# Kernel optimization log

Measured on AMD Instinct MI355X. Metric: run time of the kernel, lower is better.

The kernel has to match this reference:

```python
import jax, jax.numpy as jnp
import numpy as np

B, L, R, A, E = 256, 64, 1024, 512, 1024


def lstm_cell(x, h, c, W_ih, W_hh, b_ih, b_hh):
    # PyTorch LSTMCell gate order: i, f, g, o
    gates = x @ W_ih.T + b_ih + h @ W_hh.T + b_hh
    i, f, g, o = jnp.split(gates, 4, axis=1)
    c2 = jax.nn.sigmoid(f) * c + jax.nn.sigmoid(i) * jnp.tanh(g)
    h2 = jax.nn.sigmoid(o) * jnp.tanh(c2)
    return h2, c2


def attend(h, wh_w, wh_b, wa_w, wa_b, feats_proj, feats_value):
    # Bahdanau attention: tanh(Wh h + proj(feats)) -> scalar logit -> softmax -> weighted sum
    dot = jnp.tanh(feats_proj + (h @ wh_w.T + wh_b)[:, None, :])  # [B,L,A]
    logits = jnp.einsum('bla,a->bl', dot, wa_w[0]) + wa_b[0]      # [B,L]
    w = jax.nn.softmax(logits, axis=1)
    return jnp.einsum('bl,bld->bd', w, feats_value)


def setup_inputs() -> dict:
    key = jax.random.key(0)
    ks = iter(jax.random.split(key, 64))
    rn = lambda shape, s=1.0: jax.random.normal(next(ks), shape, dtype=jnp.float32) * s
    inp = {
        'xt': rn((B, E)),
        'fc_feats': rn((B, R)),
        'roi_feats': rn((B, L, R)),
        'p_roi_feats': rn((B, L, A)),
        'context_feats': rn((B, L, R)),
        'state_h': rn((2, B, R)),
        'state_c': rn((2, B, R)),
        # scco (visual) LSTM: input E + 2R
        'W_ih_v': rn((4 * R, E + 2 * R), 0.02), 'W_hh_v': rn((4 * R, R), 0.02),
        'b_ih_v': rn((4 * R,), 0.02), 'b_hh_v': rn((4 * R,), 0.02),
        # language LSTM: input 2R
        'W_ih_l': rn((4 * R, 2 * R), 0.02), 'W_hh_l': rn((4 * R, R), 0.02),
        'b_ih_l': rn((4 * R,), 0.02), 'b_hh_l': rn((4 * R,), 0.02),
        # SingleSP: wh, wa
        'sp_wh_w': rn((A, R), 0.02), 'sp_wh_b': rn((A,), 0.02),
        'sp_wa_w': rn((1, A), 0.02), 'sp_wa_b': rn((1,), 0.02),
        # ContextSP: wh, wv, wa
        'ctx_wh_w': rn((A, R), 0.02), 'ctx_wh_b': rn((A,), 0.02),
        'ctx_wv_w': rn((A, R), 0.02), 'ctx_wv_b': rn((A,), 0.02),
        'ctx_wa_w': rn((1, A), 0.02), 'ctx_wa_b': rn((1,), 0.02),
        # CompSP: wh, wv, wa
        'cmp_wh_w': rn((A, R), 0.02), 'cmp_wh_b': rn((A,), 0.02),
        'cmp_wv_w': rn((A, R), 0.02), 'cmp_wv_b': rn((A,), 0.02),
        'cmp_wa_w': rn((1, A), 0.02), 'cmp_wa_b': rn((1,), 0.02),
        # OutputSP: wv, wh, wa
        'out_wv_w': rn((A, R), 0.02), 'out_wv_b': rn((A,), 0.02),
        'out_wh_w': rn((A, R), 0.02), 'out_wh_b': rn((A,), 0.02),
        'out_wa_w': rn((1, A), 0.02), 'out_wa_b': rn((1,), 0.02),
    }
    return inp


def reference(xt, fc_feats, roi_feats, p_roi_feats, context_feats, state_h, state_c,
              W_ih_v, W_hh_v, b_ih_v, b_hh_v, W_ih_l, W_hh_l, b_ih_l, b_hh_l,
              sp_wh_w, sp_wh_b, sp_wa_w, sp_wa_b,
              ctx_wh_w, ctx_wh_b, ctx_wv_w, ctx_wv_b, ctx_wa_w, ctx_wa_b,
              cmp_wh_w, cmp_wh_b, cmp_wv_w, cmp_wv_b, cmp_wa_w, cmp_wa_b,
              out_wv_w, out_wv_b, out_wh_w, out_wh_b, out_wa_w, out_wa_b):
    prev_h = state_h[-1]
    env = jnp.concatenate([prev_h, fc_feats, xt], axis=1)  # [B, 2R+E]
    h_vis, c_vis = lstm_cell(env, state_h[0], state_c[0], W_ih_v, W_hh_v, b_ih_v, b_hh_v)

    # SingleSP: attend over rois using precomputed projections p_roi_feats
    single_feat = attend(h_vis, sp_wh_w, sp_wh_b, sp_wa_w, sp_wa_b, p_roi_feats, roi_feats)

    # ContextSP: attend over context_feats
    ctx_proj = context_feats @ ctx_wv_w.T + ctx_wv_b
    context_feat = attend(h_vis, ctx_wh_w, ctx_wh_b, ctx_wa_w, ctx_wa_b, ctx_proj, context_feats)

    # CompSP: attend over relation feats = context - roi
    rel = context_feat[:, None, :] - roi_feats  # [B,L,R]
    rel_proj = rel @ cmp_wv_w.T + cmp_wv_b
    comp_feat = attend(h_vis, cmp_wh_w, cmp_wh_b, cmp_wa_w, cmp_wa_b, rel_proj, rel)

    # OutputSP: attend over {single, comp, fc}
    feats3 = jnp.stack([single_feat, comp_feat, fc_feats], axis=1)  # [B,3,R]
    f3_proj = feats3 @ out_wv_w.T + out_wv_b
    output_feats = attend(h_vis, out_wh_w, out_wh_b, out_wa_w, out_wa_b, f3_proj, feats3)

    lang_in = jnp.concatenate([output_feats, h_vis], axis=1)  # [B,2R]
    h_lang, c_lang = lstm_cell(lang_in, state_h[1], state_c[1], W_ih_l, W_hh_l, b_ih_l, b_hh_l)

    output = h_lang  # dropout is identity in eval mode
    new_h = jnp.stack([h_vis, h_lang])
    new_c = jnp.stack([c_vis, c_lang])
    return output, new_h, new_c, output_feats
```

## Files before the change

### kernel.cpp

```cpp
#include <hip/hip_runtime.h>
#include <hip/hip_bf16.h>
#include <math.h>

#define B_ 256
#define L_ 64
#define R_ 1024
#define A_ 512
#define E_ 1024
#define BR (B_ * R_)

typedef __attribute__((ext_vector_type(8))) short short8;
typedef __attribute__((ext_vector_type(4))) float f32x4;

__device__ __forceinline__ unsigned int pkbf(float x, float y) {
    union { __hip_bfloat162 h; unsigned int u; } cv;
    cv.h = __float22bfloat162_rn(make_float2(x, y));
    return cv.u;
}

__device__ __forceinline__ float tanh_fast(float x) {
    return 1.f - 2.f / (1.f + __expf(2.f * x));
}
__device__ __forceinline__ float sigm_(float x) { return 1.f / (1.f + __expf(-x)); }

__device__ __forceinline__ void mm_core(const float* __restrict__ Abm, int lda,
                                        const float* __restrict__ Wbn, int ldw,
                                        int K, f32x4 acc[4][4])
{
    __shared__ unsigned int As[2048];
    __shared__ unsigned int Ws[2048];

    const int t = threadIdx.x;
    const int srow = t >> 3;
    const int sub = t & 7;
    const int q = sub >> 1, half = sub & 1;
    const int csw = (q ^ ((srow >> 1) & 3));
    int sidx[4];
    const float* pa[4];
    const float* pw[4];
    #pragma unroll
    for (int i = 0; i < 4; ++i) {
        int row = srow + 32 * i;
        sidx[i] = row * 16 + csw * 4 + half * 2;
        pa[i] = Abm + (size_t)row * lda + sub * 4;
        pw[i] = Wbn + (size_t)row * ldw + sub * 4;
    }

    const int w = t >> 6, lane = t & 63;
    const int m0 = (w >> 1) * 64, n0 = (w & 1) * 64;
    const int lrow = lane & 15, quad = lane >> 4;
    int aidx[4], widx[4];
    #pragma unroll
    for (int i = 0; i < 4; ++i) {
        int ra = m0 + i * 16 + lrow;
        aidx[i] = ra * 16 + ((quad ^ ((ra >> 1) & 3)) << 2);
        int rw = n0 + i * 16 + lrow;
        widx[i] = rw * 16 + ((quad ^ ((rw >> 1) & 3)) << 2);
    }

    for (int k0 = 0; k0 < K; k0 += 32) {
        #pragma unroll
        for (int i = 0; i < 4; ++i) {
            float4 av = *(const float4*)pa[i]; pa[i] += 32;
            float4 wv = *(const float4*)pw[i]; pw[i] += 32;
            *(uint2*)(As + sidx[i]) = make_uint2(pkbf(av.x, av.y), pkbf(av.z, av.w));
            *(uint2*)(Ws + sidx[i]) = make_uint2(pkbf(wv.x, wv.y), pkbf(wv.z, wv.w));
        }
        __syncthreads();
        short8 af[4], wf[4];
        #pragma unroll
        for (int i = 0; i < 4; ++i) {
            af[i] = *(const short8*)(As + aidx[i]);
            wf[i] = *(const short8*)(Ws + widx[i]);
        }
        #pragma unroll
        for (int mt = 0; mt < 4; ++mt)
            #pragma unroll
            for (int nt = 0; nt < 4; ++nt)
                acc[mt][nt] = __builtin_amdgcn_mfma_f32_16x16x32_bf16(
                    af[mt], wf[nt], acc[mt][nt], 0, 0, 0);
        __syncthreads();
    }
}

__device__ __forceinline__ void mm_store(f32x4 acc[4][4], float* Cbm, int ldc,
                                         int bn, const float* bias)
{
    const int t = threadIdx.x;
    const int w = t >> 6, lane = t & 63;
    const int m0 = (w >> 1) * 64, n0 = (w & 1) * 64;
    const int lrow = lane & 15, quad = lane >> 4;
    #pragma unroll
    for (int nt = 0; nt < 4; ++nt) {
        int col = bn + n0 + nt * 16 + lrow;
        float bv = bias ? bias[col] : 0.f;
        #pragma unroll
        for (int mt = 0; mt < 4; ++mt) {
            int rbase = m0 + mt * 16 + quad * 4;
            #pragma unroll
            for (int r = 0; r < 4; ++r)
                Cbm[(size_t)(rbase + r) * ldc + col] = acc[mt][nt][r] + bv;
        }
    }
}

__global__ __launch_bounds__(256) void mm_plain(
    const float* __restrict__ A, int lda, const float* __restrict__ W, int ldw,
    const float* __restrict__ bias, float* __restrict__ C, int ldc, int K,
    int M1, const float* __restrict__ A2, const float* __restrict__ bias2,
    float* __restrict__ C2)
{
    int bm = blockIdx.y * 128, bn = blockIdx.x * 128;
    const float* Abm; float* Cbm; const float* bs;
    if (bm < M1) {
        Abm = A + (size_t)bm * lda; Cbm = C + (size_t)bm * ldc; bs = bias;
    } else {
        int bm2 = bm - M1;
        Abm = A2 + (size_t)bm2 * lda; Cbm = C2 + (size_t)bm2 * ldc; bs = bias2;
    }
    f32x4 acc[4][4];
    #pragma unroll
    for (int i = 0; i < 4; ++i)
        #pragma unroll
        for (int j = 0; j < 4; ++j) acc[i][j] = (f32x4)0.f;
    mm_core(Abm, lda, W + (size_t)bn * ldw, ldw, K, acc);
    mm_store(acc, Cbm, ldc, bn, bs);
}

struct P4 { const float* W[4]; const float* bias[4]; };
__global__ __launch_bounds__(256) void mm_batch4(
    const float* __restrict__ A, int lda, P4 p, float* __restrict__ Cbase,
    int ldc, int K, int zstride)
{
    int z = blockIdx.z;
    int bm = blockIdx.y * 128, bn = blockIdx.x * 128;
    f32x4 acc[4][4];
    #pragma unroll
    for (int i = 0; i < 4; ++i)
        #pragma unroll
        for (int j = 0; j < 4; ++j) acc[i][j] = (f32x4)0.f;
    mm_core(A + (size_t)bm * lda, lda, p.W[z] + (size_t)bn * lda, lda, K, acc);
    mm_store(acc, Cbase + (size_t)z * zstride + (size_t)bm * ldc, ldc, bn, p.bias[z]);
}

struct C4 { const float* A[4]; const float* W[4]; int lda[4]; int ldw[4]; };
__global__ __launch_bounds__(256) void mm_chunks(
    C4 p, float* __restrict__ Cbase, int ldc, int K, int zstride)
{
    int z = blockIdx.z;
    int bm = blockIdx.y * 128, bn = blockIdx.x * 128;
    f32x4 acc[4][4];
    #pragma unroll
    for (int i = 0; i < 4; ++i)
        #pragma unroll
        for (int j = 0; j < 4; ++j) acc[i][j] = (f32x4)0.f;
    mm_core(p.A[z] + (size_t)bm * p.lda[z], p.lda[z],
            p.W[z] + (size_t)bn * p.ldw[z], p.ldw[z], K, acc);
    mm_store(acc, Cbase + (size_t)z * zstride + (size_t)bm * ldc, ldc, bn, nullptr);
}

__global__ void build_env(const float* __restrict__ prev_h,
                          const float* __restrict__ fc,
                          const float* __restrict__ xt,
                          float* __restrict__ env)
{
    int idx = blockIdx.x * blockDim.x + threadIdx.x;
    int b = idx / 3072, k = idx - b * 3072;
    float v;
    if (k < R_)          v = prev_h[b * R_ + k];
    else if (k < 2 * R_) v = fc[b * R_ + (k - R_)];
    else                 v = xt[b * E_ + (k - 2 * R_)];
    env[idx] = v;
}

__global__ void build_lang_in(const float* __restrict__ of,
                              const float* __restrict__ hv,
                              float* __restrict__ li)
{
    int idx = blockIdx.x * blockDim.x + threadIdx.x;
    int b = idx >> 11, k = idx & 2047;
    li[idx] = (k < R_) ? of[b * R_ + k] : hv[b * R_ + (k - R_)];
}

__global__ void build_feats3(const float* __restrict__ sf,
                             const float* __restrict__ cf,
                             const float* __restrict__ fc,
                             float* __restrict__ f3)
{
    int idx = blockIdx.x * blockDim.x + threadIdx.x;
    int d = idx % R_;
    int tt = idx / R_;
    int j = tt % 3, b = tt / 3;
    float v;
    if (j == 0)      v = sf[b * R_ + d];
    else if (j == 1) v = cf[b * R_ + d];
    else             v = fc[b * R_ + d];
    f3[idx] = v;
}

__global__ void lstm_pw(const float* __restrict__ gp, int P,
                        const float* __restrict__ b_ih, const float* __restrict__ b_hh,
                        const float* __restrict__ c_prev,
                        float* __restrict__ h_out, float* __restrict__ h_out2,
                        float* __restrict__ c_out)
{
    int idx = blockIdx.x * blockDim.x + threadIdx.x;
    int b = idx >> 10, r = idx & (R_ - 1);
    float g[4];
    #pragma unroll
    for (int gi = 0; gi < 4; ++gi) {
        int o = gi * R_ + r;
        float s = b_ih[o] + b_hh[o];
        for (int p = 0; p < P; ++p)
            s += gp[(size_t)p * B_ * 4096 + (size_t)b * 4096 + o];
        g[gi] = s;
    }
    float c2 = sigm_(g[1]) * c_prev[idx] + sigm_(g[0]) * tanh_fast(g[2]);
    float h2 = sigm_(g[3]) * tanh_fast(c2);
    c_out[idx] = c2;
    h_out[idx] = h2;
    if (h_out2) h_out2[idx] = h2;
}

__global__ __launch_bounds__(256) void attn_logits(
    const float* __restrict__ base, const float* __restrict__ base2,
    const float* __restrict__ proj,
    const float* __restrict__ wa, const float* __restrict__ wa_b,
    float* __restrict__ logits, int L, float sign)
{
    int idx = blockIdx.x * 4 + (threadIdx.x >> 6);
    int lane = threadIdx.x & 63;
    int b = idx / L;
    const float* p = proj + (size_t)idx * A_;
    const float* bs = base + (size_t)b * A_;
    const float* bs2 = base2 ? base2 + (size_t)b * A_ : nullptr;
    float acc = 0.f;
    #pragma unroll
    for (int a0 = 0; a0 < A_; a0 += 64) {
        int a = a0 + lane;
        float bb = bs[a];
        if (bs2) bb += bs2[a];
        acc += tanh_fast(bb + sign * p[a]) * wa[a];
    }
    #pragma unroll
    for (int off = 32; off > 0; off >>= 1) acc += __shfl_xor(acc, off);
    if (lane == 0) logits[idx] = acc + wa_b[0];
}

__global__ __launch_bounds__(256) void softmax_rows(
    const float* __restrict__ logits, float* __restrict__ w, int L)
{
    int row = blockIdx.x * 4 + (threadIdx.x >> 6);
    int lane = threadIdx.x & 63;
    float v = (lane < L) ? logits[row * L + lane] : -INFINITY;
    float m = v;
    #pragma unroll
    for (int off = 32; off > 0; off >>= 1) m = fmaxf(m, __shfl_xor(m, off));
    float e = (lane < L) ? __expf(v - m) : 0.f;
    float s = e;
    #pragma unroll
    for (int off = 32; off > 0; off >>= 1) s += __shfl_xor(s, off);
    if (lane < L) w[row * L + lane] = e / s;
}

__global__ void weighted_sum(const float* __restrict__ w,
                             const float* __restrict__ V,
                             const float* __restrict__ addfrom,
                             float* __restrict__ out, int L, int D)
{
    int idx = blockIdx.x * blockDim.x + threadIdx.x;
    int b = idx / D, d = idx - b * D;
    const float* vp = V + (size_t)b * L * D + d;
    const float* wp = w + b * L;
    float acc = 0.f;
    for (int l = 0; l < L; ++l) acc += wp[l] * vp[(size_t)l * D];
    out[idx] = addfrom ? (addfrom[idx] - acc) : acc;
}

extern "C" void kernel_launch(void* const* d_in, const int* in_sizes, int n_in,
                              void* d_out, int out_size, void* d_ws, size_t ws_size,
                              hipStream_t stream)
{
    const float* xt      = (const float*)d_in[0];
    const float* fc      = (const float*)d_in[1];
    const float* roi     = (const float*)d_in[2];
    const float* p_roi   = (const float*)d_in[3];
    const float* ctxf    = (const float*)d_in[4];
    const float* sh      = (const float*)d_in[5];
    const float* sc      = (const float*)d_in[6];
    const float* W_ih_v  = (const float*)d_in[7];
    const float* W_hh_v  = (const float*)d_in[8];
    const float* b_ih_v  = (const float*)d_in[9];
    const float* b_hh_v  = (const float*)d_in[10];
    const float* W_ih_l  = (const float*)d_in[11];
    const float* W_hh_l  = (const float*)d_in[12];
    const float* b_ih_l  = (const float*)d_in[13];
    const float* b_hh_l  = (const float*)d_in[14];
    const float* sp_wh_w = (const float*)d_in[15];
    const float* sp_wh_b = (const float*)d_in[16];
    const float* sp_wa_w = (const float*)d_in[17];
    const float* sp_wa_b = (const float*)d_in[18];
    const float* ctx_wh_w= (const float*)d_in[19];
    const float* ctx_wh_b= (const float*)d_in[20];
    const float* ctx_wv_w= (const float*)d_in[21];
    const float* ctx_wv_b= (const float*)d_in[22];
    const float* ctx_wa_w= (const float*)d_in[23];
    const float* ctx_wa_b= (const float*)d_in[24];
    const float* cmp_wh_w= (const float*)d_in[25];
    const float* cmp_wh_b= (const float*)d_in[26];
    const float* cmp_wv_w= (const float*)d_in[27];
    const float* cmp_wv_b= (const float*)d_in[28];
    const float* cmp_wa_w= (const float*)d_in[29];
    const float* cmp_wa_b= (const float*)d_in[30];
    const float* out_wv_w= (const float*)d_in[31];
    const float* out_wv_b= (const float*)d_in[32];
    const float* out_wh_w= (const float*)d_in[33];
    const float* out_wh_b= (const float*)d_in[34];
    const float* out_wa_w= (const float*)d_in[35];
    const float* out_wa_b= (const float*)d_in[36];

    float* out = (float*)d_out;
    float* h_vis    = out + BR;
    float* h_lang   = out;
    float* h_lang2  = out + 2 * BR;
    float* c_vis    = out + 3 * BR;
    float* c_lang   = out + 4 * BR;
    float* out_feats= out + 5 * BR;

    float* ws = (float*)d_ws;
    float* env        = ws;
    float* proj_big   = env + (size_t)B_ * 3072;
    float* gates      = proj_big;
    float* hproj4     = proj_big + (size_t)16384 * A_;
    float* base_cmp2  = hproj4 + (size_t)4 * B_ * A_;
    float* logits     = base_cmp2 + (size_t)B_ * A_;
    float* attw       = logits + B_ * L_;
    float* single_feat= attw + B_ * L_;
    float* context_feat = single_feat + BR;
    float* comp_feat  = context_feat + BR;
    float* feats3     = comp_feat + BR;
    float* f3_proj    = feats3 + (size_t)B_ * 3 * R_;
    float* lang_in    = f3_proj + (size_t)768 * A_;

    const dim3 blk(256);
    const int HUGE_M = 1 << 30;

    build_env<<<dim3(B_ * 3072 / 256), blk, 0, stream>>>(sh + BR, fc, xt, env);
    {
        C4 cv;
        cv.A[0] = env;        cv.lda[0] = 3072; cv.W[0] = W_ih_v;        cv.ldw[0] = 3072;
        cv.A[1] = env + 1024; cv.lda[1] = 3072; cv.W[1] = W_ih_v + 1024; cv.ldw[1] = 3072;
        cv.A[2] = env + 2048; cv.lda[2] = 3072; cv.W[2] = W_ih_v + 2048; cv.ldw[2] = 3072;
        cv.A[3] = sh;         cv.lda[3] = 1024; cv.W[3] = W_hh_v;        cv.ldw[3] = 1024;
        mm_chunks<<<dim3(32, 2, 4), blk, 0, stream>>>(cv, gates, 4096, 1024, B_ * 4096);
    }
    lstm_pw<<<dim3(BR / 256), blk, 0, stream>>>(gates, 4, b_ih_v, b_hh_v, sc, h_vis, nullptr, c_vis);

    {
        P4 p;
        p.W[0] = sp_wh_w;  p.bias[0] = sp_wh_b;
        p.W[1] = ctx_wh_w; p.bias[1] = ctx_wh_b;
        p.W[2] = cmp_wh_w; p.bias[2] = cmp_wh_b;
        p.W[3] = out_wh_w; p.bias[3] = out_wh_b;
        mm_batch4<<<dim3(4, 2, 4), blk, 0, stream>>>(h_vis, 1024, p, hproj4, 512, 1024, B_ * A_);
    }

    attn_logits<<<dim3(B_ * L_ / 4), blk, 0, stream>>>(hproj4, nullptr, p_roi, sp_wa_w, sp_wa_b, logits, L_, 1.f);
    softmax_rows<<<dim3(B_ / 4), blk, 0, stream>>>(logits, attw, L_);
    weighted_sum<<<dim3(BR / 256), blk, 0, stream>>>(attw, roi, nullptr, single_feat, L_, R_);

    mm_plain<<<dim3(4, 128), blk, 0, stream>>>(ctxf, 1024, ctx_wv_w, 1024, ctx_wv_b,
                                               proj_big, 512, 1024, HUGE_M, nullptr, nullptr, nullptr);
    attn_logits<<<dim3(B_ * L_ / 4), blk, 0, stream>>>(hproj4 + (size_t)B_ * A_, nullptr, proj_big,
                                                       ctx_wa_w, ctx_wa_b, logits, L_, 1.f);
    softmax_rows<<<dim3(B_ / 4), blk, 0, stream>>>(logits, attw, L_);
    weighted_sum<<<dim3(BR / 256), blk, 0, stream>>>(attw, ctxf, nullptr, context_feat, L_, R_);

    mm_plain<<<dim3(4, 130), blk, 0, stream>>>(roi, 1024, cmp_wv_w, 1024, nullptr,
                                               proj_big, 512, 1024, 16384,
                                               context_feat, cmp_wv_b, base_cmp2);
    attn_logits<<<dim3(B_ * L_ / 4), blk, 0, stream>>>(hproj4 + (size_t)2 * B_ * A_, base_cmp2, proj_big,
                                                       cmp_wa_w, cmp_wa_b, logits, L_, -1.f);
    softmax_rows<<<dim3(B_ / 4), blk, 0, stream>>>(logits, attw, L_);
    weighted_sum<<<dim3(BR / 256), blk, 0, stream>>>(attw, roi, context_feat, comp_feat, L_, R_);

    build_feats3<<<dim3(B_ * 3 * R_ / 256), blk, 0, stream>>>(single_feat, comp_feat, fc, feats3);
    mm_plain<<<dim3(4, 6), blk, 0, stream>>>(feats3, 1024, out_wv_w, 1024, out_wv_b,
                                             f3_proj, 512, 1024, HUGE_M, nullptr, nullptr, nullptr);
    attn_logits<<<dim3(B_ * 3 / 4), blk, 0, stream>>>(hproj4 + (size_t)3 * B_ * A_, nullptr, f3_proj,
                                                      out_wa_w, out_wa_b, logits, 3, 1.f);
    softmax_rows<<<dim3(B_ / 4), blk, 0, stream>>>(logits, attw, 3);
    weighted_sum<<<dim3(BR / 256), blk, 0, stream>>>(attw, feats3, nullptr, out_feats, 3, R_);

    build_lang_in<<<dim3(B_ * 2048 / 256), blk, 0, stream>>>(out_feats, h_vis, lang_in);
    {
        C4 cl;
        cl.A[0] = lang_in;        cl.lda[0] = 2048; cl.W[0] = W_ih_l;        cl.ldw[0] = 2048;
        cl.A[1] = lang_in + 1024; cl.lda[1] = 2048; cl.W[1] = W_ih_l + 1024; cl.ldw[1] = 2048;
        cl.A[2] = sh + BR;        cl.lda[2] = 1024; cl.W[2] = W_hh_l;        cl.ldw[2] = 1024;
        cl.A[3] = sh + BR;        cl.lda[3] = 1024; cl.W[3] = W_hh_l;        cl.ldw[3] = 1024;
        mm_chunks<<<dim3(32, 2, 3), blk, 0, stream>>>(cl, gates, 4096, 1024, B_ * 4096);
    }
    lstm_pw<<<dim3(BR / 256), blk, 0, stream>>>(gates, 3, b_ih_l, b_hh_l, sc + BR, h_lang, h_lang2, c_lang);
}
```

Measured before the change: 718.3 us.

## Fuse attention logits into projection GEMMs, double-buffer LDS, split-K LSTM GEMMs

The GEMM core now double-buffers shared memory and prefetches the next K-slice into registers, so each iteration needs one barrier instead of two. The big context and relation projection GEMMs gain an epilogue that applies tanh and the wa dot product directly, writing per-column-tile partial logits. This removes the 16384x512 projection writes and their re-reads. The concatenation kernels are dropped in favour of split-K segments that read the inputs in place. Weighted sums are vectorised, and roi is read once to produce both the single and comp features. The cost is more partial-sum buffers and extra reduction work in lstm_pw and softmax.

```diff
diff --git a/kernel.cpp b/kernel.cpp
--- a/kernel.cpp
+++ b/kernel.cpp
@@ -27,30 +27,28 @@
                                         const float* __restrict__ Wbn, int ldw,
                                         int K, f32x4 acc[4][4])
 {
-    __shared__ unsigned int As[2048];
-    __shared__ unsigned int Ws[2048];
+    __shared__ unsigned int As[2][2048];
+    __shared__ unsigned int Ws[2][2048];
 
     const int t = threadIdx.x;
-    const int srow = t >> 3;
-    const int sub = t & 7;
-    const int q = sub >> 1, half = sub & 1;
-    const int csw = (q ^ ((srow >> 1) & 3));
+    const int srow = t >> 3, sub = t & 7;
+    const int half = sub & 1;
+    const int csw = (sub >> 1) ^ ((srow >> 1) & 3);
     int sidx[4];
     const float* pa[4];
     const float* pw[4];
-    #pragma unroll
+#pragma unroll
     for (int i = 0; i < 4; ++i) {
         int row = srow + 32 * i;
         sidx[i] = row * 16 + csw * 4 + half * 2;
         pa[i] = Abm + (size_t)row * lda + sub * 4;
         pw[i] = Wbn + (size_t)row * ldw + sub * 4;
     }
-
     const int w = t >> 6, lane = t & 63;
     const int m0 = (w >> 1) * 64, n0 = (w & 1) * 64;
     const int lrow = lane & 15, quad = lane >> 4;
     int aidx[4], widx[4];
-    #pragma unroll
+#pragma unroll
     for (int i = 0; i < 4; ++i) {
         int ra = m0 + i * 16 + lrow;
         aidx[i] = ra * 16 + ((quad ^ ((ra >> 1) & 3)) << 2);
@@ -58,144 +56,254 @@
         widx[i] = rw * 16 + ((quad ^ ((rw >> 1) & 3)) << 2);
     }
 
-    for (int k0 = 0; k0 < K; k0 += 32) {
-        #pragma unroll
-        for (int i = 0; i < 4; ++i) {
-            float4 av = *(const float4*)pa[i]; pa[i] += 32;
-            float4 wv = *(const float4*)pw[i]; pw[i] += 32;
-            *(uint2*)(As + sidx[i]) = make_uint2(pkbf(av.x, av.y), pkbf(av.z, av.w));
-            *(uint2*)(Ws + sidx[i]) = make_uint2(pkbf(wv.x, wv.y), pkbf(wv.z, wv.w));
-        }
+    float4 ra4[4], rw4[4];
+#define MMC_LOAD() do { _Pragma("unroll") for (int i = 0; i < 4; ++i) { \
+        ra4[i] = *(const float4*)pa[i]; rw4[i] = *(const float4*)pw[i]; \
+        pa[i] += 32; pw[i] += 32; } } while (0)
+#define MMC_STORE(buf) do { _Pragma("unroll") for (int i = 0; i < 4; ++i) { \
+        *(uint2*)(As[buf] + sidx[i]) = make_uint2(pkbf(ra4[i].x, ra4[i].y), pkbf(ra4[i].z, ra4[i].w)); \
+        *(uint2*)(Ws[buf] + sidx[i]) = make_uint2(pkbf(rw4[i].x, rw4[i].y), pkbf(rw4[i].z, rw4[i].w)); } } while (0)
+
+    const int n = K >> 5;
+    MMC_LOAD();
+    MMC_STORE(0);
+    MMC_LOAD();
+    for (int k = 0; k < n; ++k) {
         __syncthreads();
         short8 af[4], wf[4];
-        #pragma unroll
+#pragma unroll
         for (int i = 0; i < 4; ++i) {
-            af[i] = *(const short8*)(As + aidx[i]);
-            wf[i] = *(const short8*)(Ws + widx[i]);
+            af[i] = *(const short8*)(As[k & 1] + aidx[i]);
+            wf[i] = *(const short8*)(Ws[k & 1] + widx[i]);
         }
-        #pragma unroll
+        if (k + 1 < n) {
+            MMC_STORE((k + 1) & 1);
+            if (k + 2 < n) MMC_LOAD();
+        }
+#pragma unroll
         for (int mt = 0; mt < 4; ++mt)
-            #pragma unroll
+#pragma unroll
             for (int nt = 0; nt < 4; ++nt)
                 acc[mt][nt] = __builtin_amdgcn_mfma_f32_16x16x32_bf16(
                     af[mt], wf[nt], acc[mt][nt], 0, 0, 0);
-        __syncthreads();
-    }
-}
-
-__device__ __forceinline__ void mm_store(f32x4 acc[4][4], float* Cbm, int ldc,
-                                         int bn, const float* bias)
+    }
+#undef MMC_LOAD
+#undef MMC_STORE
+}
+
+__device__ __forceinline__ void mm_store(f32x4 acc[4][4], float* __restrict__ Cbm,
+                                         int ldc, int bn, const float* __restrict__ bias)
 {
     const int t = threadIdx.x;
     const int w = t >> 6, lane = t & 63;
     const int m0 = (w >> 1) * 64, n0 = (w & 1) * 64;
     const int lrow = lane & 15, quad = lane >> 4;
-    #pragma unroll
+#pragma unroll
     for (int nt = 0; nt < 4; ++nt) {
         int col = bn + n0 + nt * 16 + lrow;
         float bv = bias ? bias[col] : 0.f;
-        #pragma unroll
+#pragma unroll
         for (int mt = 0; mt < 4; ++mt) {
             int rbase = m0 + mt * 16 + quad * 4;
-            #pragma unroll
+#pragma unroll
             for (int r = 0; r < 4; ++r)
                 Cbm[(size_t)(rbase + r) * ldc + col] = acc[mt][nt][r] + bv;
         }
     }
 }
 
-__global__ __launch_bounds__(256) void mm_plain(
-    const float* __restrict__ A, int lda, const float* __restrict__ W, int ldw,
-    const float* __restrict__ bias, float* __restrict__ C, int ldc, int K,
-    int M1, const float* __restrict__ A2, const float* __restrict__ bias2,
-    float* __restrict__ C2)
-{
-    int bm = blockIdx.y * 128, bn = blockIdx.x * 128;
-    const float* Abm; float* Cbm; const float* bs;
-    if (bm < M1) {
-        Abm = A + (size_t)bm * lda; Cbm = C + (size_t)bm * ldc; bs = bias;
-    } else {
-        int bm2 = bm - M1;
-        Abm = A2 + (size_t)bm2 * lda; Cbm = C2 + (size_t)bm2 * ldc; bs = bias2;
-    }
-    f32x4 acc[4][4];
-    #pragma unroll
-    for (int i = 0; i < 4; ++i)
-        #pragma unroll
-        for (int j = 0; j < 4; ++j) acc[i][j] = (f32x4)0.f;
-    mm_core(Abm, lda, W + (size_t)bn * ldw, ldw, K, acc);
-    mm_store(acc, Cbm, ldc, bn, bs);
-}
-
-struct P4 { const float* W[4]; const float* bias[4]; };
-__global__ __launch_bounds__(256) void mm_batch4(
-    const float* __restrict__ A, int lda, P4 p, float* __restrict__ Cbase,
-    int ldc, int K, int zstride)
+__device__ __forceinline__ void attn_epilogue(
+    f32x4 acc[4][4], int bm, int bn, int M, int L,
+    const float* __restrict__ base, const float* __restrict__ base2,
+    const float* __restrict__ wbias, const float* __restrict__ wa,
+    float sign, float* __restrict__ lpart)
+{
+    __shared__ float lsum[2][128];
+    const int t = threadIdx.x;
+    const int w = t >> 6, lane = t & 63;
+    const int m0 = (w >> 1) * 64, n0 = (w & 1) * 64;
+    const int lrow = lane & 15, quad = lane >> 4;
+    float wav[4], wbv[4];
+    int colv[4];
+#pragma unroll
+    for (int nt = 0; nt < 4; ++nt) {
+        colv[nt] = bn + n0 + nt * 16 + lrow;
+        wav[nt] = wa[colv[nt]];
+        wbv[nt] = wbias ? wbias[colv[nt]] : 0.f;
+    }
+#pragma unroll
+    for (int mt = 0; mt < 4; ++mt) {
+#pragma unroll
+        for (int r = 0; r < 4; ++r) {
+            int rl = m0 + mt * 16 + quad * 4 + r;
+            int row = bm + rl;
+            int b = row / L;
+            const float* bp = base + (size_t)b * A_;
+            const float* bp2 = base2 ? base2 + (size_t)b * A_ : nullptr;
+            float s = 0.f;
+#pragma unroll
+            for (int nt = 0; nt < 4; ++nt) {
+                float v = bp[colv[nt]] + wbv[nt] + sign * acc[mt][nt][r];
+                if (bp2) v += bp2[colv[nt]];
+                s += tanh_fast(v) * wav[nt];
+            }
+            s += __shfl_xor(s, 1);
+            s += __shfl_xor(s, 2);
+            s += __shfl_xor(s, 4);
+            s += __shfl_xor(s, 8);
+            if (lrow == 0) lsum[w & 1][rl] = s;
+        }
+    }
+    __syncthreads();
+    if (t < 128)
+        lpart[(size_t)(bn >> 7) * M + bm + t] = lsum[0][t] + lsum[1][t];
+}
+
+struct Seg8 { const float* A[8]; const float* W[8]; int lda[8]; int ldw[8]; };
+
+__global__ __launch_bounds__(256) void mm_seg(Seg8 s, float* __restrict__ Cbase,
+                                              int ldc, int kchunk, int zstride)
 {
     int z = blockIdx.z;
     int bm = blockIdx.y * 128, bn = blockIdx.x * 128;
     f32x4 acc[4][4];
-    #pragma unroll
+#pragma unroll
     for (int i = 0; i < 4; ++i)
-        #pragma unroll
+#pragma unroll
         for (int j = 0; j < 4; ++j) acc[i][j] = (f32x4)0.f;
-    mm_core(A + (size_t)bm * lda, lda, p.W[z] + (size_t)bn * lda, lda, K, acc);
-    mm_store(acc, Cbase + (size_t)z * zstride + (size_t)bm * ldc, ldc, bn, p.bias[z]);
-}
-
-struct C4 { const float* A[4]; const float* W[4]; int lda[4]; int ldw[4]; };
-__global__ __launch_bounds__(256) void mm_chunks(
-    C4 p, float* __restrict__ Cbase, int ldc, int K, int zstride)
+    mm_core(s.A[z] + (size_t)bm * s.lda[z], s.lda[z],
+            s.W[z] + (size_t)bn * s.ldw[z], s.ldw[z], kchunk, acc);
+    mm_store(acc, Cbase + (size_t)z * zstride + (size_t)bm * ldc, ldc, bn, nullptr);
+}
+
+struct Jobs4 { const float* A[4]; const float* W[4]; const float* bias[4]; float* C[4]; };
+__global__ __launch_bounds__(256) void mm_jobs(Jobs4 p, int K)
 {
     int z = blockIdx.z;
     int bm = blockIdx.y * 128, bn = blockIdx.x * 128;
     f32x4 acc[4][4];
-    #pragma unroll
+#pragma unroll
     for (int i = 0; i < 4; ++i)
-        #pragma unroll
+#pragma unroll
         for (int j = 0; j < 4; ++j) acc[i][j] = (f32x4)0.f;
-    mm_core(p.A[z] + (size_t)bm * p.lda[z], p.lda[z],
-            p.W[z] + (size_t)bn * p.ldw[z], p.ldw[z], K, acc);
-    mm_store(acc, Cbase + (size_t)z * zstride + (size_t)bm * ldc, ldc, bn, nullptr);
-}
-
-__global__ void build_env(const float* __restrict__ prev_h,
-                          const float* __restrict__ fc,
-                          const float* __restrict__ xt,
-                          float* __restrict__ env)
+    mm_core(p.A[z] + (size_t)bm * 1024, 1024, p.W[z] + (size_t)bn * 1024, 1024, K, acc);
+    mm_store(acc, p.C[z] + (size_t)bm * 512, 512, bn, p.bias[z]);
+}
+
+__global__ __launch_bounds__(256) void mm_fused_attn(
+    const float* __restrict__ A, int lda, const float* __restrict__ W, int ldw, int K,
+    const float* __restrict__ base, const float* __restrict__ base2,
+    const float* __restrict__ wbias, const float* __restrict__ wa,
+    float sign, int M, int L, float* __restrict__ lpart)
+{
+    int bm = blockIdx.y * 128, bn = blockIdx.x * 128;
+    f32x4 acc[4][4];
+#pragma unroll
+    for (int i = 0; i < 4; ++i)
+#pragma unroll
+        for (int j = 0; j < 4; ++j) acc[i][j] = (f32x4)0.f;
+    mm_core(A + (size_t)bm * lda, lda, W + (size_t)bn * ldw, ldw, K, acc);
+    attn_epilogue(acc, bm, bn, M, L, base, base2, wbias, wa, sign, lpart);
+}
+
+__global__ __launch_bounds__(256) void attn_logits_sp(
+    const float* __restrict__ base, const float* __restrict__ proj,
+    const float* __restrict__ wa, float* __restrict__ logits)
+{
+    int idx = blockIdx.x * 4 + (threadIdx.x >> 6);
+    int lane = threadIdx.x & 63;
+    int b = idx >> 6;
+    const f32x4* p = (const f32x4*)(proj + (size_t)idx * A_);
+    const f32x4* bs = (const f32x4*)(base + (size_t)b * A_);
+    const f32x4* wv = (const f32x4*)wa;
+    float acc = 0.f;
+#pragma unroll
+    for (int i = 0; i < 2; ++i) {
+        int a = i * 64 + lane;
+        f32x4 pv = p[a], bv = bs[a], w4 = wv[a];
+#pragma unroll
+        for (int j = 0; j < 4; ++j) acc += tanh_fast(bv[j] + pv[j]) * w4[j];
+    }
+#pragma unroll
+    for (int off = 32; off > 0; off >>= 1) acc += __shfl_xor(acc, off);
+    if (lane == 0) logits[idx] = acc;
+}
+
+__global__ __launch_bounds__(256) void softmax_part(
+    const float* __restrict__ lpart, int np, int M, int L, float* __restrict__ attw)
+{
+    int grp = blockIdx.x * 4 + (threadIdx.x >> 6);
+    int lane = threadIdx.x & 63;
+    int row = grp * L + lane;
+    float v = -INFINITY;
+    if (lane < L) {
+        float s = 0.f;
+        for (int p = 0; p < np; ++p) s += lpart[(size_t)p * M + row];
+        v = s;
+    }
+    float m = v;
+#pragma unroll
+    for (int off = 32; off > 0; off >>= 1) m = fmaxf(m, __shfl_xor(m, off));
+    float e = (lane < L) ? __expf(v - m) : 0.f;
+    float s = e;
+#pragma unroll
+    for (int off = 32; off > 0; off >>= 1) s += __shfl_xor(s, off);
+    if (lane < L) attw[row] = e / s;
+}
+
+__global__ void ws_one(const float* __restrict__ wgt, const float* __restrict__ V,
+                       float* __restrict__ out)
 {
     int idx = blockIdx.x * blockDim.x + threadIdx.x;
-    int b = idx / 3072, k = idx - b * 3072;
-    float v;
-    if (k < R_)          v = prev_h[b * R_ + k];
-    else if (k < 2 * R_) v = fc[b * R_ + (k - R_)];
-    else                 v = xt[b * E_ + (k - 2 * R_)];
-    env[idx] = v;
-}
-
-__global__ void build_lang_in(const float* __restrict__ of,
-                              const float* __restrict__ hv,
-                              float* __restrict__ li)
+    int b = idx >> 8, d4 = idx & 255;
+    const f32x4* vp = (const f32x4*)(V + (size_t)b * L_ * R_) + d4;
+    const float* wp = wgt + b * L_;
+    f32x4 acc = (f32x4)0.f;
+    for (int l = 0; l < L_; ++l) acc += wp[l] * vp[(size_t)l * 256];
+    ((f32x4*)out)[idx] = acc;
+}
+
+__global__ void ws_dual(const float* __restrict__ w1, const float* __restrict__ w2,
+                        const float* __restrict__ V, const float* __restrict__ ctx,
+                        float* __restrict__ out1, float* __restrict__ out2)
 {
     int idx = blockIdx.x * blockDim.x + threadIdx.x;
-    int b = idx >> 11, k = idx & 2047;
-    li[idx] = (k < R_) ? of[b * R_ + k] : hv[b * R_ + (k - R_)];
-}
-
-__global__ void build_feats3(const float* __restrict__ sf,
-                             const float* __restrict__ cf,
-                             const float* __restrict__ fc,
-                             float* __restrict__ f3)
+    int b = idx >> 8, d4 = idx & 255;
+    const f32x4* vp = (const f32x4*)(V + (size_t)b * L_ * R_) + d4;
+    const float* p1 = w1 + b * L_;
+    const float* p2 = w2 + b * L_;
+    f32x4 a1 = (f32x4)0.f, a2 = (f32x4)0.f;
+    for (int l = 0; l < L_; ++l) {
+        f32x4 v = vp[(size_t)l * 256];
+        a1 += p1[l] * v;
+        a2 += p2[l] * v;
+    }
+    ((f32x4*)out1)[idx] = a1;
+    ((f32x4*)out2)[idx] = ((const f32x4*)ctx)[idx] - a2;
+}
+
+__global__ void ws_out_k(const float* __restrict__ wgt, const float* __restrict__ f3,
+                         float* __restrict__ out)
 {
     int idx = blockIdx.x * blockDim.x + threadIdx.x;
-    int d = idx % R_;
-    int tt = idx / R_;
+    int b = idx >> 8, d4 = idx & 255;
+    const f32x4* fp = (const f32x4*)f3;
+    f32x4 acc = (f32x4)0.f;
+#pragma unroll
+    for (int j = 0; j < 3; ++j)
+        acc += wgt[b * 3 + j] * fp[(size_t)(b * 3 + j) * 256 + d4];
+    ((f32x4*)out)[idx] = acc;
+}
+
+__global__ void build_feats3(const float* __restrict__ sf, const float* __restrict__ cf,
+                             const float* __restrict__ fc, float* __restrict__ f3)
+{
+    int idx = blockIdx.x * blockDim.x + threadIdx.x;
+    int d4 = idx & 255;
+    int tt = idx >> 8;
     int j = tt % 3, b = tt / 3;
-    float v;
-    if (j == 0)      v = sf[b * R_ + d];
-    else if (j == 1) v = cf[b * R_ + d];
-    else             v = fc[b * R_ + d];
-    f3[idx] = v;
+    const float* src = (j == 0) ? sf : (j == 1) ? cf : fc;
+    ((f32x4*)f3)[idx] = ((const f32x4*)(src + (size_t)b * R_))[d4];
 }
 
 __global__ void lstm_pw(const float* __restrict__ gp, int P,
@@ -205,76 +313,27 @@
                         float* __restrict__ c_out)
 {
     int idx = blockIdx.x * blockDim.x + threadIdx.x;
-    int b = idx >> 10, r = idx & (R_ - 1);
-    float g[4];
-    #pragma unroll
+    int b = idx >> 8, r4 = idx & 255;
+    f32x4 g[4];
+#pragma unroll
     for (int gi = 0; gi < 4; ++gi) {
-        int o = gi * R_ + r;
-        float s = b_ih[o] + b_hh[o];
+        int o = gi * 256 + r4;
+        f32x4 s = ((const f32x4*)b_ih)[o] + ((const f32x4*)b_hh)[o];
         for (int p = 0; p < P; ++p)
-            s += gp[(size_t)p * B_ * 4096 + (size_t)b * 4096 + o];
+            s += ((const f32x4*)(gp + (size_t)p * B_ * 4096 + (size_t)b * 4096))[o];
         g[gi] = s;
     }
-    float c2 = sigm_(g[1]) * c_prev[idx] + sigm_(g[0]) * tanh_fast(g[2]);
-    float h2 = sigm_(g[3]) * tanh_fast(c2);
-    c_out[idx] = c2;
-    h_out[idx] = h2;
-    if (h_out2) h_out2[idx] = h2;
-}
-
-__global__ __launch_bounds__(256) void attn_logits(
-    const float* __restrict__ base, const float* __restrict__ base2,
-    const float* __restrict__ proj,
-    const float* __restrict__ wa, const float* __restrict__ wa_b,
-    float* __restrict__ logits, int L, float sign)
-{
-    int idx = blockIdx.x * 4 + (threadIdx.x >> 6);
-    int lane = threadIdx.x & 63;
-    int b = idx / L;
-    const float* p = proj + (size_t)idx * A_;
-    const float* bs = base + (size_t)b * A_;
-    const float* bs2 = base2 ? base2 + (size_t)b * A_ : nullptr;
-    float acc = 0.f;
-    #pragma unroll
-    for (int a0 = 0; a0 < A_; a0 += 64) {
-        int a = a0 + lane;
-        float bb = bs[a];
-        if (bs2) bb += bs2[a];
-        acc += tanh_fast(bb + sign * p[a]) * wa[a];
-    }
-    #pragma unroll
-    for (int off = 32; off > 0; off >>= 1) acc += __shfl_xor(acc, off);
-    if (lane == 0) logits[idx] = acc + wa_b[0];
-}
-
-__global__ __launch_bounds__(256) void softmax_rows(
-    const float* __restrict__ logits, float* __restrict__ w, int L)
-{
-    int row = blockIdx.x * 4 + (threadIdx.x >> 6);
-    int lane = threadIdx.x & 63;
-    float v = (lane < L) ? logits[row * L + lane] : -INFINITY;
-    float m = v;
-    #pragma unroll
-    for (int off = 32; off > 0; off >>= 1) m = fmaxf(m, __shfl_xor(m, off));
-    float e = (lane < L) ? __expf(v - m) : 0.f;
-    float s = e;
-    #pragma unroll
-    for (int off = 32; off > 0; off >>= 1) s += __shfl_xor(s, off);
-    if (lane < L) w[row * L + lane] = e / s;
-}
-
-__global__ void weighted_sum(const float* __restrict__ w,
-                             const float* __restrict__ V,
-                             const float* __restrict__ addfrom,
-                             float* __restrict__ out, int L, int D)
-{
-    int idx = blockIdx.x * blockDim.x + threadIdx.x;
-    int b = idx / D, d = idx - b * D;
-    const float* vp = V + (size_t)b * L * D + d;
-    const float* wp = w + b * L;
-    float acc = 0.f;
-    for (int l = 0; l < L; ++l) acc += wp[l] * vp[(size_t)l * D];
-    out[idx] = addfrom ? (addfrom[idx] - acc) : acc;
+    f32x4 cp = ((const f32x4*)c_prev)[idx];
+    f32x4 c2, h2;
+#pragma unroll
+    for (int j = 0; j < 4; ++j) {
+        float cc = sigm_(g[1][j]) * cp[j] + sigm_(g[0][j]) * tanh_fast(g[2][j]);
+        c2[j] = cc;
+        h2[j] = sigm_(g[3][j]) * tanh_fast(cc);
+    }
+    ((f32x4*)c_out)[idx] = c2;
+    ((f32x4*)h_out)[idx] = h2;
+    if (h_out2) ((f32x4*)h_out2)[idx] = h2;
 }
 
 extern "C" void kernel_launch(void* const* d_in, const int* in_sizes, int n_in,
@@ -299,25 +358,21 @@
     const float* sp_wh_w = (const float*)d_in[15];
     const float* sp_wh_b = (const float*)d_in[16];
     const float* sp_wa_w = (const float*)d_in[17];
-    const float* sp_wa_b = (const float*)d_in[18];
     const float* ctx_wh_w= (const float*)d_in[19];
     const float* ctx_wh_b= (const float*)d_in[20];
     const float* ctx_wv_w= (const float*)d_in[21];
     const float* ctx_wv_b= (const float*)d_in[22];
     const float* ctx_wa_w= (const float*)d_in[23];
-    const float* ctx_wa_b= (const float*)d_in[24];
     const float* cmp_wh_w= (const float*)d_in[25];
     const float* cmp_wh_b= (const float*)d_in[26];
     const float* cmp_wv_w= (const float*)d_in[27];
     const float* cmp_wv_b= (const float*)d_in[28];
     const float* cmp_wa_w= (const float*)d_in[29];
-    const float* cmp_wa_b= (const float*)d_in[30];
     const float* out_wv_w= (const float*)d_in[31];
     const float* out_wv_b= (const float*)d_in[32];
     const float* out_wh_w= (const float*)d_in[33];
     const float* out_wh_b= (const float*)d_in[34];
     const float* out_wa_w= (const float*)d_in[35];
-    const float* out_wa_b= (const float*)d_in[36];
 
     float* out = (float*)d_out;
     float* h_vis    = out + BR;
@@ -328,78 +383,95 @@
     float* out_feats= out + 5 * BR;
 
     float* ws = (float*)d_ws;
-    float* env        = ws;
-    float* proj_big   = env + (size_t)B_ * 3072;
-    float* gates      = proj_big;
-    float* hproj4     = proj_big + (size_t)16384 * A_;
+    float* gates      = ws;
+    float* hproj4     = gates + (size_t)8 * B_ * 4096;
     float* base_cmp2  = hproj4 + (size_t)4 * B_ * A_;
-    float* logits     = base_cmp2 + (size_t)B_ * A_;
-    float* attw       = logits + B_ * L_;
-    float* single_feat= attw + B_ * L_;
+    float* lpart      = base_cmp2 + (size_t)B_ * A_;
+    float* lpart_out  = lpart + 4 * 16384;
+    float* logits_sp  = lpart_out + 4 * 768;
+    float* attw_sp    = logits_sp + 16384;
+    float* attw_ctx   = attw_sp + 16384;
+    float* attw_cmp   = attw_ctx + 16384;
+    float* attw_out   = attw_cmp + 16384;
+    float* single_feat= attw_out + 768;
     float* context_feat = single_feat + BR;
     float* comp_feat  = context_feat + BR;
     float* feats3     = comp_feat + BR;
-    float* f3_proj    = feats3 + (size_t)B_ * 3 * R_;
-    float* lang_in    = f3_proj + (size_t)768 * A_;
+
+    float* hp0 = hproj4;
+    float* hp1 = hproj4 + (size_t)B_ * A_;
+    float* hp2 = hproj4 + (size_t)2 * B_ * A_;
+    float* hp3 = hproj4 + (size_t)3 * B_ * A_;
 
     const dim3 blk(256);
-    const int HUGE_M = 1 << 30;
-
-    build_env<<<dim3(B_ * 3072 / 256), blk, 0, stream>>>(sh + BR, fc, xt, env);
+    const int ZST = B_ * 4096;
+
     {
-        C4 cv;
-        cv.A[0] = env;        cv.lda[0] = 3072; cv.W[0] = W_ih_v;        cv.ldw[0] = 3072;
-        cv.A[1] = env + 1024; cv.lda[1] = 3072; cv.W[1] = W_ih_v + 1024; cv.ldw[1] = 3072;
-        cv.A[2] = env + 2048; cv.lda[2] = 3072; cv.W[2] = W_ih_v + 2048; cv.ldw[2] = 3072;
-        cv.A[3] = sh;         cv.lda[3] = 1024; cv.W[3] = W_hh_v;        cv.ldw[3] = 1024;
-        mm_chunks<<<dim3(32, 2, 4), blk, 0, stream>>>(cv, gates, 4096, 1024, B_ * 4096);
-    }
-    lstm_pw<<<dim3(BR / 256), blk, 0, stream>>>(gates, 4, b_ih_v, b_hh_v, sc, h_vis, nullptr, c_vis);
+        Seg8 s;
+        s.A[0] = sh + BR;       s.W[0] = W_ih_v;          s.lda[0] = 1024; s.ldw[0] = 3072;
+        s.A[1] = sh + BR + 512; s.W[1] = W_ih_v + 512;    s.lda[1] = 1024; s.ldw[1] = 3072;
+        s.A[2] = fc;            s.W[2] = W_ih_v + 1024;   s.lda[2] = 1024; s.ldw[2] = 3072;
+        s.A[3] = fc + 512;      s.W[3] = W_ih_v + 1536;   s.lda[3] = 1024; s.ldw[3] = 3072;
+        s.A[4] = xt;            s.W[4] = W_ih_v + 2048;   s.lda[4] = 1024; s.ldw[4] = 3072;
+        s.A[5] = xt + 512;      s.W[5] = W_ih_v + 2560;   s.lda[5] = 1024; s.ldw[5] = 3072;
+        s.A[6] = sh;            s.W[6] = W_hh_v;          s.lda[6] = 1024; s.ldw[6] = 1024;
+        s.A[7] = sh + 512;      s.W[7] = W_hh_v + 512;    s.lda[7] = 1024; s.ldw[7] = 1024;
+        mm_seg<<<dim3(32, 2, 8), blk, 0, stream>>>(s, gates, 4096, 512, ZST);
+    }
+    lstm_pw<<<dim3(B_), blk, 0, stream>>>(gates, 8, b_ih_v, b_hh_v, sc, h_vis, nullptr, c_vis);
 
     {
-        P4 p;
-        p.W[0] = sp_wh_w;  p.bias[0] = sp_wh_b;
-        p.W[1] = ctx_wh_w; p.bias[1] = ctx_wh_b;
-        p.W[2] = cmp_wh_w; p.bias[2] = cmp_wh_b;
-        p.W[3] = out_wh_w; p.bias[3] = out_wh_b;
-        mm_batch4<<<dim3(4, 2, 4), blk, 0, stream>>>(h_vis, 1024, p, hproj4, 512, 1024, B_ * A_);
-    }
-
-    attn_logits<<<dim3(B_ * L_ / 4), blk, 0, stream>>>(hproj4, nullptr, p_roi, sp_wa_w, sp_wa_b, logits, L_, 1.f);
-    softmax_rows<<<dim3(B_ / 4), blk, 0, stream>>>(logits, attw, L_);
-    weighted_sum<<<dim3(BR / 256), blk, 0, stream>>>(attw, roi, nullptr, single_feat, L_, R_);
-
-    mm_plain<<<dim3(4, 128), blk, 0, stream>>>(ctxf, 1024, ctx_wv_w, 1024, ctx_wv_b,
-                                               proj_big, 512, 1024, HUGE_M, nullptr, nullptr, nullptr);
-    attn_logits<<<dim3(B_ * L_ / 4), blk, 0, stream>>>(hproj4 + (size_t)B_ * A_, nullptr, proj_big,
-                                                       ctx_wa_w, ctx_wa_b, logits, L_, 1.f);
-    softmax_rows<<<dim3(B_ / 4), blk, 0, stream>>>(logits, attw, L_);
-    weighted_sum<<<dim3(BR / 256), blk, 0, stream>>>(attw, ctxf, nullptr, context_feat, L_, R_);
-
-    mm_plain<<<dim3(4, 130), blk, 0, stream>>>(roi, 1024, cmp_wv_w, 1024, nullptr,
-                                               proj_big, 512, 1024, 16384,
-                                               context_feat, cmp_wv_b, base_cmp2);
-    attn_logits<<<dim3(B_ * L_ / 4), blk, 0, stream>>>(hproj4 + (size_t)2 * B_ * A_, base_cmp2, proj_big,
-                                                       cmp_wa_w, cmp_wa_b, logits, L_, -1.f);
-    softmax_rows<<<dim3(B_ / 4), blk, 0, stream>>>(logits, attw, L_);
-    weighted_sum<<<dim3(BR / 256), blk, 0, stream>>>(attw, roi, context_feat, comp_feat, L_, R_);
-
-    build_feats3<<<dim3(B_ * 3 * R_ / 256), blk, 0, stream>>>(single_feat, comp_feat, fc, feats3);
-    mm_plain<<<dim3(4, 6), blk, 0, stream>>>(feats3, 1024, out_wv_w, 1024, out_wv_b,
-                                             f3_proj, 512, 1024, HUGE_M, nullptr, nullptr, nullptr);
-    attn_logits<<<dim3(B_ * 3 / 4), blk, 0, stream>>>(hproj4 + (size_t)3 * B_ * A_, nullptr, f3_proj,
-                                                      out_wa_w, out_wa_b, logits, 3, 1.f);
-    softmax_rows<<<dim3(B_ / 4), blk, 0, stream>>>(logits, attw, 3);
-    weighted_sum<<<dim3(BR / 256), blk, 0, stream>>>(attw, feats3, nullptr, out_feats, 3, R_);
-
-    build_lang_in<<<dim3(B_ * 2048 / 256), blk, 0, stream>>>(out_feats, h_vis, lang_in);
+        Jobs4 p;
+        p.A[0] = h_vis; p.W[0] = sp_wh_w;  p.bias[0] = sp_wh_b;  p.C[0] = hp0;
+        p.A[1] = h_vis; p.W[1] = ctx_wh_w; p.bias[1] = ctx_wh_b; p.C[1] = hp1;
+        p.A[2] = h_vis; p.W[2] = cmp_wh_w; p.bias[2] = cmp_wh_b; p.C[2] = hp2;
+        p.A[3] = h_vis; p.W[3] = out_wh_w; p.bias[3] = out_wh_b; p.C[3] = hp3;
+        mm_jobs<<<dim3(4, 2, 4), blk, 0, stream>>>(p, 1024);
+    }
+
+    attn_logits_sp<<<dim3(B_ * L_ / 4), blk, 0, stream>>>(hp0, p_roi, sp_wa_w, logits_sp);
+    softmax_part<<<dim3(64), blk, 0, stream>>>(logits_sp, 1, 16384, 64, attw_sp);
+
+    mm_fused_attn<<<dim3(4, 128), blk, 0, stream>>>(ctxf, 1024, ctx_wv_w, 1024, 1024,
+                                                    hp1, nullptr, ctx_wv_b, ctx_wa_w,
+                                                    1.f, 16384, 64, lpart);
+    softmax_part<<<dim3(64), blk, 0, stream>>>(lpart, 4, 16384, 64, attw_ctx);
+    ws_one<<<dim3(B_), blk, 0, stream>>>(attw_ctx, ctxf, context_feat);
+
     {
-        C4 cl;
-        cl.A[0] = lang_in;        cl.lda[0] = 2048; cl.W[0] = W_ih_l;        cl.ldw[0] = 2048;
-        cl.A[1] = lang_in + 1024; cl.lda[1] = 2048; cl.W[1] = W_ih_l + 1024; cl.ldw[1] = 2048;
-        cl.A[2] = sh + BR;        cl.lda[2] = 1024; cl.W[2] = W_hh_l;        cl.ldw[2] = 1024;
-        cl.A[3] = sh + BR;        cl.lda[3] = 1024; cl.W[3] = W_hh_l;        cl.ldw[3] = 1024;
-        mm_chunks<<<dim3(32, 2, 3), blk, 0, stream>>>(cl, gates, 4096, 1024, B_ * 4096);
-    }
-    lstm_pw<<<dim3(BR / 256), blk, 0, stream>>>(gates, 3, b_ih_l, b_hh_l, sc + BR, h_lang, h_lang2, c_lang);
-}
+        Jobs4 p;
+        p.A[0] = p.A[1] = p.A[2] = p.A[3] = context_feat;
+        p.W[0] = p.W[1] = p.W[2] = p.W[3] = cmp_wv_w;
+        p.bias[0] = p.bias[1] = p.bias[2] = p.bias[3] = cmp_wv_b;
+        p.C[0] = p.C[1] = p.C[2] = p.C[3] = base_cmp2;
+        mm_jobs<<<dim3(4, 2, 1), blk, 0, stream>>>(p, 1024);
+    }
+    mm_fused_attn<<<dim3(4, 128), blk, 0, stream>>>(roi, 1024, cmp_wv_w, 1024, 1024,
+                                                    hp2, base_cmp2, nullptr, cmp_wa_w,
+                                                    -1.f, 16384, 64, lpart);
+    softmax_part<<<dim3(64), blk, 0, stream>>>(lpart, 4, 16384, 64, attw_cmp);
+    ws_dual<<<dim3(B_), blk, 0, stream>>>(attw_sp, attw_cmp, roi, context_feat,
+                                          single_feat, comp_feat);
+
+    build_feats3<<<dim3(B_ * 3), blk, 0, stream>>>(single_feat, comp_feat, fc, feats3);
+    mm_fused_attn<<<dim3(4, 6), blk, 0, stream>>>(feats3, 1024, out_wv_w, 1024, 1024,
+                                                  hp3, nullptr, out_wv_b, out_wa_w,
+                                                  1.f, 768, 3, lpart_out);
+    softmax_part<<<dim3(64), blk, 0, stream>>>(lpart_out, 4, 768, 3, attw_out);
+    ws_out_k<<<dim3(B_), blk, 0, stream>>>(attw_out, feats3, out_feats);
+
+    {
+        Seg8 s;
+        s.A[0] = out_feats;       s.W[0] = W_ih_l;        s.lda[0] = 1024; s.ldw[0] = 2048;
+        s.A[1] = out_feats + 512; s.W[1] = W_ih_l + 512;  s.lda[1] = 1024; s.ldw[1] = 2048;
+        s.A[2] = h_vis;           s.W[2] = W_ih_l + 1024; s.lda[2] = 1024; s.ldw[2] = 2048;
+        s.A[3] = h_vis + 512;     s.W[3] = W_ih_l + 1536; s.lda[3] = 1024; s.ldw[3] = 2048;
+        s.A[4] = sh + BR;         s.W[4] = W_hh_l;        s.lda[4] = 1024; s.ldw[4] = 1024;
+        s.A[5] = sh + BR + 512;   s.W[5] = W_hh_l + 512;  s.lda[5] = 1024; s.ldw[5] = 1024;
+        s.A[6] = s.A[5];          s.W[6] = s.W[5];        s.lda[6] = 1024; s.ldw[6] = 1024;
+        s.A[7] = s.A[5];          s.W[7] = s.W[5];        s.lda[7] = 1024; s.ldw[7] = 1024;
+        mm_seg<<<dim3(32, 2, 6), blk, 0, stream>>>(s, gates, 4096, 512, ZST);
+    }
+    lstm_pw<<<dim3(B_), blk, 0, stream>>>(gates, 6, b_ih_l, b_hh_l, sc + BR,
+                                          h_lang, h_lang2, c_lang);
+}
```

New measurement: 587.5 us. -18.2%, faster.
